# Kernel tuning notes

Hardware: AMD Instinct MI355X
Metric: run time of the kernel (lower is better)

The kernel has to match this reference:

```python
import jax, jax.numpy as jnp
import numpy as np

B, N, VF, EF, DV, DE, LN = 64, 64, 32, 16, 128, 128, 4
EPS_INNER = 128.0  # BatchNorm1d(MAX_N, internal_d_vert): 2nd positional arg is eps (faithful to source bug)
EPS_BN = 1e-5


def gev_layer(v_in, e_in, evW, evb, eW, eb, vW, vb, relu=True):
    act = jax.nn.relu if relu else (lambda x: x)
    ev = v_in @ evW + evb                                   # [B,N,De]
    # outer_v_sum: ev.unsqueeze(1) + ev.unsqueeze(2) -> [B,N,N,De]
    e_out = act(e_in @ eW + eb + ev[:, None, :, :] + ev[:, :, None, :])
    per_v_e = e_out.sum(axis=1)                             # sum-aggregate over dim 1
    v_out = act(jnp.concatenate([per_v_e, v_in], axis=-1) @ vW + vb)
    return v_out, e_out


def bn_flat(v, g, b):
    # BatchNorm1d(N*VF) on [B, N*VF] in training mode (biased var)
    x = v.reshape(-1, N * VF)
    mu = x.mean(axis=0)
    var = x.var(axis=0)
    x = (x - mu) * jax.lax.rsqrt(var + EPS_BN) * g + b
    return x.reshape(-1, N, VF)


def bn_inner(v, g, b):
    # BatchNorm1d(MAX_N, eps=128) on [B, N, D]: channels are the N axis, stats over (B, D)
    mu = v.mean(axis=(0, 2), keepdims=True)
    var = v.var(axis=(0, 2), keepdims=True)
    return (v - mu) * jax.lax.rsqrt(var + EPS_INNER) * g[None, :, None] + b[None, :, None]


def setup_inputs() -> dict:
    key = jax.random.key(0)
    ks = jax.random.split(key, 24)
    s = 0.01  # force_lin_init with init_noise=0.01, biases zero
    nrm = lambda k, shp: jax.random.normal(k, shp, dtype=jnp.float32) * s
    inp = {
        "v": jax.random.normal(ks[0], (B, N, VF), dtype=jnp.float32),
        "e": jax.random.normal(ks[1], (B, N, N, EF), dtype=jnp.float32),
        "bn_in_g": jnp.ones((N * VF,), jnp.float32),
        "bn_in_b": jnp.zeros((N * VF,), jnp.float32),
        "g1_evW": nrm(ks[2], (VF, DE)), "g1_evb": jnp.zeros((DE,), jnp.float32),
        "g1_eW": nrm(ks[3], (EF, DE)), "g1_eb": jnp.zeros((DE,), jnp.float32),
        "g1_vW": nrm(ks[4], (VF + DE, DV)), "g1_vb": jnp.zeros((DV,), jnp.float32),
        "inn_evW": nrm(ks[5], (LN, DV, DE)), "inn_evb": jnp.zeros((LN, DE), jnp.float32),
        "inn_eW": nrm(ks[6], (LN, DE, DE)), "inn_eb": jnp.zeros((LN, DE), jnp.float32),
        "inn_vW": nrm(ks[7], (LN, DV + DE, DV)), "inn_vb": jnp.zeros((LN, DV), jnp.float32),
        "bn_g": jnp.ones((LN, N), jnp.float32),
        "bn_b": jnp.zeros((LN, N), jnp.float32),
        "g3_evW": nrm(ks[8], (DV, 1)), "g3_evb": jnp.zeros((1,), jnp.float32),
        "g3_eW": nrm(ks[9], (DE, 1)), "g3_eb": jnp.zeros((1,), jnp.float32),
        "g3_vW": nrm(ks[10], (DV + 1, 1)), "g3_vb": jnp.zeros((1,), jnp.float32),
    }
    return inp


def reference(v, e, bn_in_g, bn_in_b, g1_evW, g1_evb, g1_eW, g1_eb, g1_vW, g1_vb,
              inn_evW, inn_evb, inn_eW, inn_eb, inn_vW, inn_vb, bn_g, bn_b,
              g3_evW, g3_evb, g3_eW, g3_eb, g3_vW, g3_vb):
    v = bn_flat(v, bn_in_g, bn_in_b)
    v, e = gev_layer(v, e, g1_evW, g1_evb, g1_eW, g1_eb, g1_vW, g1_vb)
    for i in range(LN):
        v_next, e_next = gev_layer(v, e, inn_evW[i], inn_evb[i], inn_eW[i], inn_eb[i], inn_vW[i], inn_vb[i])
        v = v_next + v  # resnet
        e = e_next + e
        v = bn_inner(v, bn_g[i], bn_b[i])
    v, e = gev_layer(v, e, g3_evW, g3_evb, g3_eW, g3_eb, g3_vW, g3_vb, relu=False)
    return v, e
```

## Files before the change

### kernel.cpp

```cpp
#include <hip/hip_runtime.h>
#include <hip/hip_bf16.h>


typedef __bf16 bf16_t;
typedef __bf16 bf16x8 __attribute__((ext_vector_type(8)));
typedef __bf16 bf16x4 __attribute__((ext_vector_type(4)));
typedef __bf16 bf16x2 __attribute__((ext_vector_type(2)));
typedef float f32x4 __attribute__((ext_vector_type(4)));

__device__ __forceinline__ void bar_lgkm() {
  asm volatile("s_waitcnt lgkmcnt(0)\n\ts_barrier" ::: "memory");
}

__device__ __forceinline__ unsigned pack2(float a, float b) {
  bf16_t ba = (bf16_t)a, bb = (bf16_t)b;
  unsigned short ua, ub;
  __builtin_memcpy(&ua, &ba, 2);
  __builtin_memcpy(&ub, &bb, 2);
  return (unsigned)ua | ((unsigned)ub << 16);
}
__device__ __forceinline__ float blo(unsigned u) {
  unsigned v = u << 16; float f; __builtin_memcpy(&f, &v, 4); return f;
}
__device__ __forceinline__ float bhi(unsigned u) {
  unsigned v = u & 0xffff0000u; float f; __builtin_memcpy(&f, &v, 4); return f;
}

__global__ __launch_bounds__(256) void k_prep(const float* __restrict__ vin,
    const float* __restrict__ g, const float* __restrict__ bt,
    const float* __restrict__ eW, const float* __restrict__ inn_vW,
    const float* __restrict__ g1_vW, const float* __restrict__ inn_evW,
    float* __restrict__ v0, bf16_t* __restrict__ Wt, float* __restrict__ stats,
    unsigned* __restrict__ vWp, unsigned* __restrict__ g1_vWp,
    unsigned* __restrict__ evWp, bf16_t* __restrict__ evWtB) {
  const int blk = blockIdx.x, tid = threadIdx.x;
  if (blk < 8) {
    int ch = blk * 256 + tid;
    float s = 0.f, s2 = 0.f;
    for (int b = 0; b < 64; ++b) { float x = vin[b * 2048 + ch]; s += x; s2 += x * x; }
    float mu = s * (1.f / 64.f);
    float var = s2 * (1.f / 64.f) - mu * mu;
    float sc = rsqrtf(var + 1e-5f) * g[ch];
    float bb = bt[ch];
    for (int b = 0; b < 64; ++b) {
      float x = vin[b * 2048 + ch];
      v0[b * 2048 + ch] = (x - mu) * sc + bb;
    }
  } else if (blk < 264) {
    int idx = (blk - 8) * 256 + tid;
    int l = idx >> 14, r = idx & 16383, n = r >> 7, k = r & 127;
    Wt[idx] = (bf16_t)eW[(l << 14) + (k << 7) + n];
  } else if (blk == 264) {
    for (int i = tid; i < 512; i += 256) stats[i] = 0.f;
  } else if (blk < 521) {
    int idx = (blk - 265) * 256 + tid;
    int l = idx >> 14, r = idx & 16383;
    int k8 = r >> 9, c = (r >> 2) & 127, j = r & 3;
    int ka = k8 * 8 + j * 2;
    vWp[idx] = pack2(inn_vW[(l << 15) + ka * 128 + c],
                     inn_vW[(l << 15) + (ka + 1) * 128 + c]);
  } else if (blk < 561) {
    int idx = (blk - 521) * 256 + tid;
    int k8 = idx >> 9, c = (idx >> 2) & 127, j = idx & 3;
    int ka = k8 * 8 + j * 2;
    g1_vWp[idx] = pack2(g1_vW[ka * 128 + c], g1_vW[(ka + 1) * 128 + c]);
  } else if (blk < 689) {
    int idx = (blk - 561) * 256 + tid;
    int l = idx >> 13, r = idx & 8191;
    int k8 = r >> 9, c = (r >> 2) & 127, j = r & 3;
    int ka = k8 * 8 + j * 2;
    evWp[idx] = pack2(inn_evW[(l << 14) + ka * 128 + c],
                      inn_evW[(l << 14) + (ka + 1) * 128 + c]);
  } else {
    int idx = (blk - 689) * 256 + tid;
    int l = idx >> 14, r = idx & 16383, n = r >> 7, k = r & 127;
    evWtB[idx] = (bf16_t)inn_evW[(l << 14) + (k << 7) + n];
  }
}

template <int K>
__global__ __launch_bounds__(256) void k_ev(const float* __restrict__ v_in,
    const float* __restrict__ W, const float* __restrict__ bias,
    float* __restrict__ out) {
  __shared__ float rows_s[8][K];
  const int r0 = blockIdx.x * 8;
  const int tid = threadIdx.x;
  const int c = tid & 127, h = tid >> 7;
  for (int idx = tid; idx < 8 * K; idx += 256) {
    int rr = idx / K, kk = idx % K;
    rows_s[rr][kk] = v_in[(r0 + rr) * K + kk];
  }
  __syncthreads();
  float acc[4];
  const float bv = bias[c];
#pragma unroll
  for (int r = 0; r < 4; ++r) acc[r] = bv;
  for (int k4 = 0; k4 < K; k4 += 4) {
    float w0 = W[(k4 + 0) * 128 + c], w1 = W[(k4 + 1) * 128 + c];
    float w2 = W[(k4 + 2) * 128 + c], w3 = W[(k4 + 3) * 128 + c];
#pragma unroll
    for (int r = 0; r < 4; ++r) {
      float4 x = *(const float4*)&rows_s[h * 4 + r][k4];
      acc[r] += x.x * w0 + x.y * w1 + x.z * w2 + x.w * w3;
    }
  }
#pragma unroll
  for (int r = 0; r < 4; ++r) out[(r0 + h * 4 + r) * 128 + c] = acc[r];
}

__global__ __launch_bounds__(256) void k_edge_g1(const float* __restrict__ e0,
    const float* __restrict__ eW, const float* __restrict__ eb,
    const float* __restrict__ evA, bf16_t* __restrict__ e_ws,
    const float* __restrict__ v0, const uint4* __restrict__ g1_vWp,
    const float* __restrict__ vb, const uint4* __restrict__ evW0p,
    const float* __restrict__ evb, float* __restrict__ v,
    float* __restrict__ evB) {
  __shared__ bf16_t A0s[2][64][40];
  __shared__ bf16_t Os[2][64][136];
  __shared__ float in_s[2][160];
  __shared__ float vr_s[2][128];
  __shared__ float red[2][2][128];
  const int b = blockIdx.x >> 5, j0 = (blockIdx.x & 31) * 2;
  const int tid = threadIdx.x;
  const int lane = tid & 63, w = tid >> 6;
  const int quad = lane >> 4, l16 = lane & 15;
  f32x4 v0reg;
  if (tid < 16)
    v0reg = *(const f32x4*)&v0[(b * 64 + j0 + (tid >> 3)) * 32 + (tid & 7) * 4];
#pragma unroll
  for (int t = 0; t < 2; ++t) {
    int idx = tid + t * 256;
    int row = idx >> 3, off = (idx & 7) * 4;
    int jc = off >> 4, k = off & 15;
    f32x4 x = *(const f32x4*)&e0[((b * 64 + row) * 64 + j0) * 16 + off];
    bf16x4 y;
#pragma unroll
    for (int r = 0; r < 4; ++r) y[r] = (bf16_t)x[r];
    *(bf16x4*)&A0s[jc][row][k] = y;
    bf16x4 z = {(bf16_t)0.f, (bf16_t)0.f, (bf16_t)0.f, (bf16_t)0.f};
    *(bf16x4*)&A0s[jc][row][16 + k] = z;
  }
  const int c0[2] = {w * 32 + quad * 4, w * 32 + 16 + quad * 4};
  bf16x8 wf[2];
#pragma unroll
  for (int nt = 0; nt < 2; ++nt) {
    const int c = w * 32 + nt * 16 + l16;
#pragma unroll
    for (int jj = 0; jj < 8; ++jj)
      wf[nt][jj] = (quad < 2) ? (bf16_t)eW[(quad * 8 + jj) * 128 + c] : (bf16_t)0.f;
  }
  f32x4 acc[2][4][2];
  {
    f32x4 ebv[2], evj[2][2], evi[4][2];
#pragma unroll
    for (int nt = 0; nt < 2; ++nt) {
      ebv[nt] = *(const f32x4*)&eb[c0[nt]];
#pragma unroll
      for (int jc = 0; jc < 2; ++jc)
        evj[jc][nt] = *(const f32x4*)&evA[(b * 64 + j0 + jc) * 128 + c0[nt]];
#pragma unroll
      for (int mt = 0; mt < 4; ++mt)
        evi[mt][nt] = *(const f32x4*)&evA[(b * 64 + mt * 16 + l16) * 128 + c0[nt]];
    }
#pragma unroll
    for (int jc = 0; jc < 2; ++jc)
#pragma unroll
      for (int mt = 0; mt < 4; ++mt)
#pragma unroll
        for (int nt = 0; nt < 2; ++nt)
          acc[jc][mt][nt] = ebv[nt] + evj[jc][nt] + evi[mt][nt];
  }
  __syncthreads();
#pragma unroll
  for (int jc = 0; jc < 2; ++jc) {
#pragma unroll
    for (int mt = 0; mt < 4; ++mt) {
      bf16x8 ef = *(const bf16x8*)&A0s[jc][mt * 16 + l16][quad * 8];
#pragma unroll
      for (int nt = 0; nt < 2; ++nt)
        acc[jc][mt][nt] = __builtin_amdgcn_mfma_f32_16x16x32_bf16(wf[nt], ef, acc[jc][mt][nt], 0, 0, 0);
    }
  }
#pragma unroll
  for (int jc = 0; jc < 2; ++jc) {
#pragma unroll
    for (int nt = 0; nt < 2; ++nt) {
      f32x4 ps = {0.f, 0.f, 0.f, 0.f};
#pragma unroll
      for (int mt = 0; mt < 4; ++mt) {
        const int i = mt * 16 + l16;
        bf16x4 outv;
#pragma unroll
        for (int r = 0; r < 4; ++r) {
          float vv = fmaxf(acc[jc][mt][nt][r], 0.f);
          ps[r] += vv;
          outv[r] = (bf16_t)vv;
        }
        *(bf16x4*)&Os[jc][i][c0[nt]] = outv;
      }
#pragma unroll
      for (int m = 1; m <= 8; m <<= 1) {
#pragma unroll
        for (int r = 0; r < 4; ++r) ps[r] += __shfl_xor(ps[r], m);
      }
      if (l16 == 0) *(f32x4*)&in_s[jc][c0[nt]] = ps;
    }
  }
  if (tid < 16) *(f32x4*)&in_s[tid >> 3][128 + (tid & 7) * 4] = v0reg;
  __syncthreads();
  {
    bf16_t* ebase = &e_ws[((size_t)(b * 64 + j0) * 64) * 128];
#pragma unroll
    for (int t = 0; t < 8; ++t) {
      int idx = tid + t * 256;
      *(int4*)&ebase[idx * 8] =
          *(const int4*)&Os[idx >> 10][(idx >> 4) & 63][(idx & 15) * 8];
    }
  }
  const int khalf = w >> 1, cbase = (w & 1) << 6;
  const int cc = cbase + lane;
  const int c = tid & 127, h = tid >> 7;
  {
    float p0 = 0.f, p1 = 0.f;
    const uint4* Wp = &g1_vWp[(khalf * 10) * 128 + cc];
    const float* xs0 = &in_s[0][khalf * 80];
    const float* xs1 = &in_s[1][khalf * 80];
#pragma unroll 5
    for (int k8 = 0; k8 < 10; ++k8) {
      uint4 wv = Wp[k8 * 128];
      float we0 = blo(wv.x), wo0 = bhi(wv.x);
      float we1 = blo(wv.y), wo1 = bhi(wv.y);
      float we2 = blo(wv.z), wo2 = bhi(wv.z);
      float we3 = blo(wv.w), wo3 = bhi(wv.w);
      float4 xa0 = *(const float4*)&xs0[k8 * 8];
      float4 xb0 = *(const float4*)&xs0[k8 * 8 + 4];
      float4 xa1 = *(const float4*)&xs1[k8 * 8];
      float4 xb1 = *(const float4*)&xs1[k8 * 8 + 4];
      p0 += xa0.x * we0 + xa0.y * wo0 + xa0.z * we1 + xa0.w * wo1
          + xb0.x * we2 + xb0.y * wo2 + xb0.z * we3 + xb0.w * wo3;
      p1 += xa1.x * we0 + xa1.y * wo0 + xa1.z * we1 + xa1.w * wo1
          + xb1.x * we2 + xb1.y * wo2 + xb1.z * we3 + xb1.w * wo3;
    }
    red[khalf][0][cc] = p0;
    red[khalf][1][cc] = p1;
  }
  bar_lgkm();
  {
    float vacc = vb[c] + red[0][h][c] + red[1][h][c];
    float vr = fmaxf(vacc, 0.f);
    v[(b * 64 + j0 + h) * 128 + c] = vr;
    vr_s[h][c] = vr;
  }
  bar_lgkm();
  {
    float p0 = 0.f, p1 = 0.f;
    const uint4* Wp = &evW0p[(khalf * 8) * 128 + cc];
    const float* xs0 = &vr_s[0][khalf << 6];
    const float* xs1 = &vr_s[1][khalf << 6];
#pragma unroll 4
    for (int k8 = 0; k8 < 8; ++k8) {
      uint4 wv = Wp[k8 * 128];
      float we0 = blo(wv.x), wo0 = bhi(wv.x);
      float we1 = blo(wv.y), wo1 = bhi(wv.y);
      float we2 = blo(wv.z), wo2 = bhi(wv.z);
      float we3 = blo(wv.w), wo3 = bhi(wv.w);
      float4 xa0 = *(const float4*)&xs0[k8 * 8];
      float4 xb0 = *(const float4*)&xs0[k8 * 8 + 4];
      float4 xa1 = *(const float4*)&xs1[k8 * 8];
      float4 xb1 = *(const float4*)&xs1[k8 * 8 + 4];
      p0 += xa0.x * we0 + xa0.y * wo0 + xa0.z * we1 + xa0.w * wo1
          + xb0.x * we2 + xb0.y * wo2 + xb0.z * we3 + xb0.w * wo3;
      p1 += xa1.x * we0 + xa1.y * wo0 + xa1.z * we1 + xa1.w * wo1
          + xb1.x * we2 + xb1.y * wo2 + xb1.z * we3 + xb1.w * wo3;
    }
    red[khalf][0][cc] = p0;
    red[khalf][1][cc] = p1;
  }
  bar_lgkm();
  evB[(b * 64 + j0 + h) * 128 + c] = evb[c] + red[0][h][c] + red[1][h][c];
}

template <bool LAST, bool EVGEN>
__global__ __launch_bounds__(256) void k_edge_inner(bf16_t* __restrict__ e_ws,
    const bf16_t* __restrict__ Wt, const float* __restrict__ eb,
    const float* __restrict__ ev, const float* __restrict__ eW3,
    float* __restrict__ edt, const float* __restrict__ vin,
    float* __restrict__ vout, const uint4* __restrict__ vWp,
    const float* __restrict__ vb, float* __restrict__ statsAcc,
    const float* __restrict__ statsPrev, const float* __restrict__ gPrev,
    const float* __restrict__ btPrev, const bf16_t* __restrict__ evWtB,
    const float* __restrict__ evb) {
  __shared__ bf16_t As[2][64][136];
  __shared__ float W3s[128];
  __shared__ float in_s[2][256];
  __shared__ float red[2][2][128];
  __shared__ float part[4][2];
  __shared__ float scs[64], shs[64];
  const int b = blockIdx.x >> 5, j0 = (blockIdx.x & 31) * 2;
  const int tid = threadIdx.x;
  const int lane = tid & 63, w = tid >> 6;
  const int quad = lane >> 4, l16 = lane & 15;
  bf16_t* ebase = &e_ws[((size_t)(b * 64 + j0) * 64) * 128];
  int4 stg[8];
#pragma unroll
  for (int t = 0; t < 8; ++t) {
    int idx = tid + t * 256;
    stg[t] = *(const int4*)&ebase[idx * 8];
  }
  f32x4 vreg;
  if (tid < 64)
    vreg = *(const f32x4*)&vin[(b * 64 + j0 + (tid >> 5)) * 128 + (tid & 31) * 4];
  if (LAST) {
    if (tid < 128) W3s[tid] = eW3[tid];
  }
  bf16x8 wf[2][4];
#pragma unroll
  for (int nt = 0; nt < 2; ++nt)
#pragma unroll
    for (int ks = 0; ks < 4; ++ks)
      wf[nt][ks] = *(const bf16x8*)&Wt[(w * 32 + nt * 16 + l16) * 128 + ks * 32 + quad * 8];
  const int c0[2] = {w * 32 + quad * 4, w * 32 + 16 + quad * 4};
  f32x4 acc[2][4][2];
  if (EVGEN) {
    if (tid < 64) {
      float mu = statsPrev[tid] * (1.f / 8192.f);
      float var = statsPrev[64 + tid] * (1.f / 8192.f) - mu * mu;
      float sc = rsqrtf(var + 128.f) * gPrev[tid];
      scs[tid] = sc;
      shs[tid] = btPrev[tid] - mu * sc;
    }
    bf16x8 wf2[2][4];
#pragma unroll
    for (int nt = 0; nt < 2; ++nt)
#pragma unroll
      for (int ks = 0; ks < 4; ++ks)
        wf2[nt][ks] = *(const bf16x8*)&evWtB[(w * 32 + nt * 16 + l16) * 128 + ks * 32 + quad * 8];
    bar_lgkm();
#pragma unroll
    for (int t = 0; t < 16; ++t) {
      int row = t * 4 + w;
      float2 xv = *(const float2*)&vin[(b * 64 + row) * 128 + lane * 2];
      float sc = scs[row], sh = shs[row];
      bf16x2 o;
      o[0] = (bf16_t)(xv.x * sc + sh);
      o[1] = (bf16_t)(xv.y * sc + sh);
      *(bf16x2*)&As[0][row][lane * 2] = o;
    }
    if (tid < 64) {
      int rr = j0 + (tid >> 5);
      vreg = vreg * scs[rr] + shs[rr];
    }
    bar_lgkm();
    f32x4 acc_ev[4][2];
#pragma unroll
    for (int nt = 0; nt < 2; ++nt) {
      f32x4 bias = *(const f32x4*)&evb[c0[nt]];
#pragma unroll
      for (int mt = 0; mt < 4; ++mt) acc_ev[mt][nt] = bias;
    }
#pragma unroll
    for (int ks = 0; ks < 4; ++ks) {
      bf16x8 bfm[4];
#pragma unroll
      for (int mt = 0; mt < 4; ++mt)
        bfm[mt] = *(const bf16x8*)&As[0][mt * 16 + l16][ks * 32 + quad * 8];
#pragma unroll
      for (int mt = 0; mt < 4; ++mt)
#pragma unroll
        for (int nt = 0; nt < 2; ++nt)
          acc_ev[mt][nt] = __builtin_amdgcn_mfma_f32_16x16x32_bf16(wf2[nt][ks], bfm[mt], acc_ev[mt][nt], 0, 0, 0);
    }
    const int mtj = j0 >> 4;
    f32x4 evrow[2];
#pragma unroll
    for (int mt = 0; mt < 4; ++mt)
      if (mtj == mt) { evrow[0] = acc_ev[mt][0]; evrow[1] = acc_ev[mt][1]; }
    f32x4 evj[2][2];
#pragma unroll
    for (int jc = 0; jc < 2; ++jc) {
      int src = (quad << 4) | ((j0 + jc) & 15);
#pragma unroll
      for (int nt = 0; nt < 2; ++nt)
#pragma unroll
        for (int r = 0; r < 4; ++r)
          evj[jc][nt][r] = __shfl(evrow[nt][r], src);
    }
#pragma unroll
    for (int nt = 0; nt < 2; ++nt) {
      f32x4 ebv = *(const f32x4*)&eb[c0[nt]];
#pragma unroll
      for (int jc = 0; jc < 2; ++jc)
#pragma unroll
        for (int mt = 0; mt < 4; ++mt)
          acc[jc][mt][nt] = ebv + evj[jc][nt] + acc_ev[mt][nt];
    }
    bar_lgkm();
  } else {
    f32x4 ebv[2], evj[2][2], evi[4][2];
#pragma unroll
    for (int nt = 0; nt < 2; ++nt) {
      ebv[nt] = *(const f32x4*)&eb[c0[nt]];
#pragma unroll
      for (int jc = 0; jc < 2; ++jc)
        evj[jc][nt] = *(const f32x4*)&ev[(b * 64 + j0 + jc) * 128 + c0[nt]];
#pragma unroll
      for (int mt = 0; mt < 4; ++mt)
        evi[mt][nt] = *(const f32x4*)&ev[(b * 64 + mt * 16 + l16) * 128 + c0[nt]];
    }
#pragma unroll
    for (int jc = 0; jc < 2; ++jc)
#pragma unroll
      for (int mt = 0; mt < 4; ++mt)
#pragma unroll
        for (int nt = 0; nt < 2; ++nt)
          acc[jc][mt][nt] = ebv[nt] + evj[jc][nt] + evi[mt][nt];
  }
#pragma unroll
  for (int t = 0; t < 8; ++t) {
    int idx = tid + t * 256;
    *(int4*)&As[idx >> 10][(idx >> 4) & 63][(idx & 15) * 8] = stg[t];
  }
  bar_lgkm();
#pragma unroll
  for (int ks = 0; ks < 4; ++ks) {
    bf16x8 ef[2][4];
#pragma unroll
    for (int jc = 0; jc < 2; ++jc)
#pragma unroll
      for (int mt = 0; mt < 4; ++mt)
        ef[jc][mt] = *(const bf16x8*)&As[jc][mt * 16 + l16][ks * 32 + quad * 8];
#pragma unroll
    for (int jc = 0; jc < 2; ++jc)
#pragma unroll
      for (int mt = 0; mt < 4; ++mt)
#pragma unroll
        for (int nt = 0; nt < 2; ++nt)
          acc[jc][mt][nt] = __builtin_amdgcn_mfma_f32_16x16x32_bf16(wf[nt][ks], ef[jc][mt], acc[jc][mt][nt], 0, 0, 0);
  }
  bar_lgkm();
#pragma unroll
  for (int jc = 0; jc < 2; ++jc) {
#pragma unroll
    for (int nt = 0; nt < 2; ++nt) {
      f32x4 ps = {0.f, 0.f, 0.f, 0.f};
#pragma unroll
      for (int mt = 0; mt < 4; ++mt) {
        const int i = mt * 16 + l16;
        bf16x4 eo = *(const bf16x4*)&As[jc][i][c0[nt]];
        bf16x4 outv;
#pragma unroll
        for (int r = 0; r < 4; ++r) {
          float vv = fmaxf(acc[jc][mt][nt][r], 0.f);
          ps[r] += vv;
          outv[r] = (bf16_t)(vv + (float)eo[r]);
        }
        *(bf16x4*)&As[jc][i][c0[nt]] = outv;
      }
#pragma unroll
      for (int m = 1; m <= 8; m <<= 1) {
#pragma unroll
        for (int r = 0; r < 4; ++r) ps[r] += __shfl_xor(ps[r], m);
      }
      if (l16 == 0) *(f32x4*)&in_s[jc][c0[nt]] = ps;
    }
  }
  if (tid < 64) *(f32x4*)&in_s[tid >> 5][128 + (tid & 31) * 4] = vreg;
  bar_lgkm();
  const int khalf = w >> 1, cbase = (w & 1) << 6;
  const int cc = cbase + lane;
  float p0 = 0.f, p1 = 0.f;
  {
    const uint4* Wp = &vWp[(khalf * 16) * 128 + cc];
    const float* xs0 = &in_s[0][khalf << 7];
    const float* xs1 = &in_s[1][khalf << 7];
#pragma unroll 4
    for (int k8 = 0; k8 < 16; ++k8) {
      uint4 wv = Wp[k8 * 128];
      float we0 = blo(wv.x), wo0 = bhi(wv.x);
      float we1 = blo(wv.y), wo1 = bhi(wv.y);
      float we2 = blo(wv.z), wo2 = bhi(wv.z);
      float we3 = blo(wv.w), wo3 = bhi(wv.w);
      float4 xa0 = *(const float4*)&xs0[k8 * 8];
      float4 xb0 = *(const float4*)&xs0[k8 * 8 + 4];
      float4 xa1 = *(const float4*)&xs1[k8 * 8];
      float4 xb1 = *(const float4*)&xs1[k8 * 8 + 4];
      p0 += xa0.x * we0 + xa0.y * wo0 + xa0.z * we1 + xa0.w * wo1
          + xb0.x * we2 + xb0.y * wo2 + xb0.z * we3 + xb0.w * wo3;
      p1 += xa1.x * we0 + xa1.y * wo0 + xa1.z * we1 + xa1.w * wo1
          + xb1.x * we2 + xb1.y * wo2 + xb1.z * we3 + xb1.w * wo3;
    }
  }
  if (!LAST) {
#pragma unroll
    for (int t = 0; t < 8; ++t) {
      int idx = tid + t * 256;
      *(int4*)&ebase[idx * 8] =
          *(const int4*)&As[idx >> 10][(idx >> 4) & 63][(idx & 15) * 8];
    }
  } else {
    const int i = tid >> 2, q = tid & 3;
#pragma unroll
    for (int jc = 0; jc < 2; ++jc) {
      float d = 0.f;
#pragma unroll
      for (int t = 0; t < 4; ++t) {
        bf16x8 x = *(const bf16x8*)&As[jc][i][q * 32 + t * 8];
#pragma unroll
        for (int u = 0; u < 8; ++u) d += (float)x[u] * W3s[q * 32 + t * 8 + u];
      }
      d += __shfl_xor(d, 1);
      d += __shfl_xor(d, 2);
      if (q == 0) edt[(b * 64 + j0 + jc) * 64 + i] = d;
    }
  }
  red[khalf][0][cc] = p0;
  red[khalf][1][cc] = p1;
  bar_lgkm();
  const int c = tid & 127, h = tid >> 7;
  float vacc = vb[c] + red[0][h][c] + red[1][h][c];
  float vnew = fmaxf(vacc, 0.f) + in_s[h][128 + c];
  vout[(b * 64 + j0 + h) * 128 + c] = vnew;
  float s = vnew, s2 = vnew * vnew;
#pragma unroll
  for (int m = 1; m <= 32; m <<= 1) {
    s += __shfl_xor(s, m);
    s2 += __shfl_xor(s2, m);
  }
  if (lane == 0) { part[w][0] = s; part[w][1] = s2; }
  bar_lgkm();
  if (tid < 2) {
    int n = j0 + tid;
    atomicAdd(&statsAcc[n], part[tid * 2][0] + part[tid * 2 + 1][0]);
    atomicAdd(&statsAcc[64 + n], part[tid * 2][1] + part[tid * 2 + 1][1]);
  }
}

__global__ __launch_bounds__(256) void k_g3(const float* __restrict__ vv,
    const float* __restrict__ stats3, const float* __restrict__ g,
    const float* __restrict__ bt, const float* __restrict__ evW3,
    const float* __restrict__ evb3, const float* __restrict__ eb3,
    const float* __restrict__ edt, const float* __restrict__ vW3,
    const float* __restrict__ vb3, float* __restrict__ out_v,
    float* __restrict__ out_e) {
  __shared__ float vbn[64][132];
  __shared__ float edts[64][68];
  __shared__ float scs[64], shs[64];
  __shared__ float W3e[128];
  __shared__ float vWs[132];
  __shared__ float ev3s[64];
  __shared__ float pj[4][64];
  const int b = blockIdx.x, tid = threadIdx.x;
  if (tid < 64) {
    float mu = stats3[tid] * (1.f / 8192.f);
    float var = stats3[64 + tid] * (1.f / 8192.f) - mu * mu;
    float sc = rsqrtf(var + 128.f) * g[tid];
    scs[tid] = sc;
    shs[tid] = bt[tid] - mu * sc;
  }
  if (tid < 128) W3e[tid] = evW3[tid];
  if (tid < 129) vWs[tid] = vW3[tid];
  __syncthreads();
#pragma unroll
  for (int t = 0; t < 8; ++t) {
    int idx = t * 1024 + tid * 4;
    int row = idx >> 7, cc = idx & 127;
    f32x4 x = *(const f32x4*)&vv[(b * 64 + row) * 128 + cc];
    *(f32x4*)&vbn[row][cc] = x * scs[row] + shs[row];
  }
#pragma unroll
  for (int t = 0; t < 4; ++t) {
    int idx = t * 1024 + tid * 4;
    int j = idx >> 6, i = idx & 63;
    *(f32x4*)&edts[j][i] = *(const f32x4*)&edt[(b * 64 + j) * 64 + i];
  }
  __syncthreads();
  {
    int i = tid >> 2, q = tid & 3;
    float d = 0.f;
#pragma unroll
    for (int u = 0; u < 32; ++u) d += vbn[i][q * 32 + u] * W3e[q * 32 + u];
    d += __shfl_xor(d, 1);
    d += __shfl_xor(d, 2);
    if (q == 0) ev3s[i] = d + evb3[0];
  }
  __syncthreads();
  {
    int q = tid >> 6, j = tid & 63;
    float s = 0.f;
    const float e3 = eb3[0];
    const float evj = ev3s[j];
#pragma unroll
    for (int r = 0; r < 16; ++r) {
      int i = q * 16 + r;
      float val = edts[j][i] + e3 + ev3s[i] + evj;
      out_e[(b * 64 + i) * 64 + j] = val;
      s += val;
    }
    pj[q][j] = s;
  }
  __syncthreads();
  {
    int n = tid >> 2, q = tid & 3;
    float d = 0.f;
#pragma unroll
    for (int u = 0; u < 32; ++u) d += vbn[n][q * 32 + u] * vWs[1 + q * 32 + u];
    d += __shfl_xor(d, 1);
    d += __shfl_xor(d, 2);
    if (q == 0) {
      float p3 = pj[0][n] + pj[1][n] + pj[2][n] + pj[3][n];
      out_v[b * 64 + n] = d + p3 * vWs[0] + vb3[0];
    }
  }
}

extern "C" void kernel_launch(void* const* d_in, const int* in_sizes, int n_in,
                              void* d_out, int out_size, void* d_ws, size_t ws_size,
                              hipStream_t stream) {
  const float* in_v    = (const float*)d_in[0];
  const float* in_e    = (const float*)d_in[1];
  const float* bn_in_g = (const float*)d_in[2];
  const float* bn_in_b = (const float*)d_in[3];
  const float* g1_evW  = (const float*)d_in[4];
  const float* g1_evb  = (const float*)d_in[5];
  const float* g1_eW   = (const float*)d_in[6];
  const float* g1_eb   = (const float*)d_in[7];
  const float* g1_vW   = (const float*)d_in[8];
  const float* g1_vb   = (const float*)d_in[9];
  const float* inn_evW = (const float*)d_in[10];
  const float* inn_evb = (const float*)d_in[11];
  const float* inn_eW  = (const float*)d_in[12];
  const float* inn_eb  = (const float*)d_in[13];
  const float* inn_vW  = (const float*)d_in[14];
  const float* inn_vb  = (const float*)d_in[15];
  const float* bn_g    = (const float*)d_in[16];
  const float* bn_b    = (const float*)d_in[17];
  const float* g3_evW  = (const float*)d_in[18];
  const float* g3_evb  = (const float*)d_in[19];
  const float* g3_eW   = (const float*)d_in[20];
  const float* g3_eb   = (const float*)d_in[21];
  const float* g3_vW   = (const float*)d_in[22];
  const float* g3_vb   = (const float*)d_in[23];

  char* ws = (char*)d_ws;
  bf16_t* e_ws = (bf16_t*)(ws);
  float* vA       = (float*)(ws + 67108864);
  float* evA      = (float*)(ws + 69206016);
  float* evB      = (float*)(ws + 71303168);
  float* v0       = (float*)(ws + 73400320);
  bf16_t* Wt      = (bf16_t*)(ws + 73924608);
  float* edt      = (float*)(ws + 74055680);
  float* stats    = (float*)(ws + 75104256);
  unsigned* vWp   = (unsigned*)(ws + 75106304);
  unsigned* g1_vWp= (unsigned*)(ws + 75368448);
  unsigned* evWp  = (unsigned*)(ws + 75409408);
  bf16_t* evWtB   = (bf16_t*)(ws + 75540480);
  float* vB       = (float*)(ws + 75671552);

  float* out_v = (float*)d_out;
  float* out_e = (float*)d_out + 4096;

  k_prep<<<945, 256, 0, stream>>>(in_v, bn_in_g, bn_in_b, inn_eW, inn_vW, g1_vW,
                                  inn_evW, v0, Wt, stats, vWp, g1_vWp, evWp, evWtB);

  k_ev<32><<<512, 256, 0, stream>>>(v0, g1_evW, g1_evb, evA);
  k_edge_g1<<<2048, 256, 0, stream>>>(in_e, g1_eW, g1_eb, evA, e_ws,
                                      v0, (const uint4*)g1_vWp, g1_vb,
                                      (const uint4*)evWp, inn_evb, vA, evB);

  float* vbufs[2] = {vA, vB};
  for (int l = 0; l < 4; ++l) {
    float* vin_l  = vbufs[l & 1];
    float* vout_l = vbufs[(l + 1) & 1];
    if (l == 0)
      k_edge_inner<false, false><<<2048, 256, 0, stream>>>(e_ws, Wt,
          inn_eb, evB, g3_eW, edt, vin_l, vout_l,
          (const uint4*)vWp, inn_vb, stats,
          nullptr, nullptr, nullptr, nullptr, nullptr);
    else if (l < 3)
      k_edge_inner<false, true><<<2048, 256, 0, stream>>>(e_ws, Wt + l * 16384,
          inn_eb + l * 128, evB, g3_eW, edt, vin_l, vout_l,
          (const uint4*)vWp + l * 4096, inn_vb + l * 128, stats + l * 128,
          stats + (l - 1) * 128, bn_g + (l - 1) * 64, bn_b + (l - 1) * 64,
          evWtB + l * 16384, inn_evb + l * 128);
    else
      k_edge_inner<true, true><<<2048, 256, 0, stream>>>(e_ws, Wt + l * 16384,
          inn_eb + l * 128, evB, g3_eW, edt, vin_l, vout_l,
          (const uint4*)vWp + l * 4096, inn_vb + l * 128, stats + l * 128,
          stats + (l - 1) * 128, bn_g + (l - 1) * 64, bn_b + (l - 1) * 64,
          evWtB + l * 16384, inn_evb + l * 128);
  }

  k_g3<<<64, 256, 0, stream>>>(vA, stats + 384, bn_g + 192, bn_b + 192,
                               g3_evW, g3_evb, g3_eb, edt, g3_vW, g3_vb,
                               out_v, out_e);
}
```

Baseline: 367.5 us.

## Process four j-rows per block with software-pipelined edge tile loads

Measured after the change: 376.1 us. +2.3%, slower.

```diff
diff --git a/kernel.cpp b/kernel.cpp
--- a/kernel.cpp
+++ b/kernel.cpp
@@ -281,7 +281,7 @@
 }
 
 template <bool LAST, bool EVGEN>
-__global__ __launch_bounds__(256) void k_edge_inner(bf16_t* __restrict__ e_ws,
+__global__ __launch_bounds__(256, 2) void k_edge_inner(bf16_t* __restrict__ e_ws,
     const bf16_t* __restrict__ Wt, const float* __restrict__ eb,
     const float* __restrict__ ev, const float* __restrict__ eW3,
     float* __restrict__ edt, const float* __restrict__ vin,
@@ -290,25 +290,24 @@
     const float* __restrict__ statsPrev, const float* __restrict__ gPrev,
     const float* __restrict__ btPrev, const bf16_t* __restrict__ evWtB,
     const float* __restrict__ evb) {
-  __shared__ bf16_t As[2][64][136];
+  __shared__ bf16_t As[2][2][64][136];
   __shared__ float W3s[128];
-  __shared__ float in_s[2][256];
+  __shared__ float in_s[2][2][256];
   __shared__ float red[2][2][128];
   __shared__ float part[4][2];
   __shared__ float scs[64], shs[64];
-  const int b = blockIdx.x >> 5, j0 = (blockIdx.x & 31) * 2;
+  const int b = blockIdx.x >> 4, j0 = (blockIdx.x & 15) * 4;
   const int tid = threadIdx.x;
   const int lane = tid & 63, w = tid >> 6;
   const int quad = lane >> 4, l16 = lane & 15;
-  bf16_t* ebase = &e_ws[((size_t)(b * 64 + j0) * 64) * 128];
+  bf16_t* ebase0 = &e_ws[((size_t)(b * 64 + j0) * 64) * 128];
+  bf16_t* ebase1 = ebase0 + 2 * 64 * 128;
   int4 stg[8];
 #pragma unroll
-  for (int t = 0; t < 8; ++t) {
-    int idx = tid + t * 256;
-    stg[t] = *(const int4*)&ebase[idx * 8];
-  }
+  for (int t = 0; t < 8; ++t)
+    stg[t] = *(const int4*)&ebase0[(tid + t * 256) * 8];
   f32x4 vreg;
-  if (tid < 64)
+  if (tid < 128)
     vreg = *(const f32x4*)&vin[(b * 64 + j0 + (tid >> 5)) * 128 + (tid & 31) * 4];
   if (LAST) {
     if (tid < 128) W3s[tid] = eW3[tid];
@@ -320,7 +319,11 @@
     for (int ks = 0; ks < 4; ++ks)
       wf[nt][ks] = *(const bf16x8*)&Wt[(w * 32 + nt * 16 + l16) * 128 + ks * 32 + quad * 8];
   const int c0[2] = {w * 32 + quad * 4, w * 32 + 16 + quad * 4};
-  f32x4 acc[2][4][2];
+  f32x4 ebv[2];
+#pragma unroll
+  for (int nt = 0; nt < 2; ++nt) ebv[nt] = *(const f32x4*)&eb[c0[nt]];
+  f32x4 acc_ev[4][2];
+  f32x4 evj[4][2];
   if (EVGEN) {
     if (tid < 64) {
       float mu = statsPrev[tid] * (1.f / 8192.f);
@@ -344,14 +347,13 @@
       bf16x2 o;
       o[0] = (bf16_t)(xv.x * sc + sh);
       o[1] = (bf16_t)(xv.y * sc + sh);
-      *(bf16x2*)&As[0][row][lane * 2] = o;
-    }
-    if (tid < 64) {
+      *(bf16x2*)&As[1][1][row][lane * 2] = o;
+    }
+    if (tid < 128) {
       int rr = j0 + (tid >> 5);
       vreg = vreg * scs[rr] + shs[rr];
     }
     bar_lgkm();
-    f32x4 acc_ev[4][2];
 #pragma unroll
     for (int nt = 0; nt < 2; ++nt) {
       f32x4 bias = *(const f32x4*)&evb[c0[nt]];
@@ -363,7 +365,7 @@
       bf16x8 bfm[4];
 #pragma unroll
       for (int mt = 0; mt < 4; ++mt)
-        bfm[mt] = *(const bf16x8*)&As[0][mt * 16 + l16][ks * 32 + quad * 8];
+        bfm[mt] = *(const bf16x8*)&As[1][1][mt * 16 + l16][ks * 32 + quad * 8];
 #pragma unroll
       for (int mt = 0; mt < 4; ++mt)
 #pragma unroll
@@ -375,51 +377,42 @@
 #pragma unroll
     for (int mt = 0; mt < 4; ++mt)
       if (mtj == mt) { evrow[0] = acc_ev[mt][0]; evrow[1] = acc_ev[mt][1]; }
-    f32x4 evj[2][2];
-#pragma unroll
-    for (int jc = 0; jc < 2; ++jc) {
-      int src = (quad << 4) | ((j0 + jc) & 15);
+#pragma unroll
+    for (int jj = 0; jj < 4; ++jj) {
+      int src = (quad << 4) | ((j0 + jj) & 15);
 #pragma unroll
       for (int nt = 0; nt < 2; ++nt)
 #pragma unroll
         for (int r = 0; r < 4; ++r)
-          evj[jc][nt][r] = __shfl(evrow[nt][r], src);
-    }
+          evj[jj][nt][r] = __shfl(evrow[nt][r], src);
+    }
+  } else {
 #pragma unroll
     for (int nt = 0; nt < 2; ++nt) {
-      f32x4 ebv = *(const f32x4*)&eb[c0[nt]];
-#pragma unroll
-      for (int jc = 0; jc < 2; ++jc)
-#pragma unroll
-        for (int mt = 0; mt < 4; ++mt)
-          acc[jc][mt][nt] = ebv + evj[jc][nt] + acc_ev[mt][nt];
-    }
-    bar_lgkm();
-  } else {
-    f32x4 ebv[2], evj[2][2], evi[4][2];
-#pragma unroll
-    for (int nt = 0; nt < 2; ++nt) {
-      ebv[nt] = *(const f32x4*)&eb[c0[nt]];
-#pragma unroll
-      for (int jc = 0; jc < 2; ++jc)
-        evj[jc][nt] = *(const f32x4*)&ev[(b * 64 + j0 + jc) * 128 + c0[nt]];
-#pragma unroll
-      for (int mt = 0; mt < 4; ++mt)
-        evi[mt][nt] = *(const f32x4*)&ev[(b * 64 + mt * 16 + l16) * 128 + c0[nt]];
-    }
-#pragma unroll
-    for (int jc = 0; jc < 2; ++jc)
-#pragma unroll
-      for (int mt = 0; mt < 4; ++mt)
-#pragma unroll
-        for (int nt = 0; nt < 2; ++nt)
-          acc[jc][mt][nt] = ebv[nt] + evj[jc][nt] + evi[mt][nt];
+#pragma unroll
+      for (int jj = 0; jj < 4; ++jj)
+        evj[jj][nt] = *(const f32x4*)&ev[(b * 64 + j0 + jj) * 128 + c0[nt]];
+#pragma unroll
+      for (int mt = 0; mt < 4; ++mt)
+        acc_ev[mt][nt] = *(const f32x4*)&ev[(b * 64 + mt * 16 + l16) * 128 + c0[nt]];
+    }
   }
 #pragma unroll
   for (int t = 0; t < 8; ++t) {
     int idx = tid + t * 256;
-    *(int4*)&As[idx >> 10][(idx >> 4) & 63][(idx & 15) * 8] = stg[t];
-  }
+    *(int4*)&As[0][idx >> 10][(idx >> 4) & 63][(idx & 15) * 8] = stg[t];
+  }
+#pragma unroll
+  for (int t = 0; t < 8; ++t)
+    stg[t] = *(const int4*)&ebase1[(tid + t * 256) * 8];
+  f32x4 acc[2][4][2];
+#pragma unroll
+  for (int jc = 0; jc < 2; ++jc)
+#pragma unroll
+    for (int mt = 0; mt < 4; ++mt)
+#pragma unroll
+      for (int nt = 0; nt < 2; ++nt)
+        acc[jc][mt][nt] = ebv[nt] + evj[jc][nt] + acc_ev[mt][nt];
   bar_lgkm();
 #pragma unroll
   for (int ks = 0; ks < 4; ++ks) {
@@ -428,7 +421,7 @@
     for (int jc = 0; jc < 2; ++jc)
 #pragma unroll
       for (int mt = 0; mt < 4; ++mt)
-        ef[jc][mt] = *(const bf16x8*)&As[jc][mt * 16 + l16][ks * 32 + quad * 8];
+        ef[jc][mt] = *(const bf16x8*)&As[0][jc][mt * 16 + l16][ks * 32 + quad * 8];
 #pragma unroll
     for (int jc = 0; jc < 2; ++jc)
 #pragma unroll
@@ -446,7 +439,7 @@
 #pragma unroll
       for (int mt = 0; mt < 4; ++mt) {
         const int i = mt * 16 + l16;
-        bf16x4 eo = *(const bf16x4*)&As[jc][i][c0[nt]];
+        bf16x4 eo = *(const bf16x4*)&As[0][jc][i][c0[nt]];
         bf16x4 outv;
 #pragma unroll
         for (int r = 0; r < 4; ++r) {
@@ -454,84 +447,160 @@
           ps[r] += vv;
           outv[r] = (bf16_t)(vv + (float)eo[r]);
         }
-        *(bf16x4*)&As[jc][i][c0[nt]] = outv;
+        *(bf16x4*)&As[0][jc][i][c0[nt]] = outv;
       }
 #pragma unroll
       for (int m = 1; m <= 8; m <<= 1) {
 #pragma unroll
         for (int r = 0; r < 4; ++r) ps[r] += __shfl_xor(ps[r], m);
       }
-      if (l16 == 0) *(f32x4*)&in_s[jc][c0[nt]] = ps;
-    }
-  }
-  if (tid < 64) *(f32x4*)&in_s[tid >> 5][128 + (tid & 31) * 4] = vreg;
+      if (l16 == 0) *(f32x4*)&in_s[0][jc][c0[nt]] = ps;
+    }
+  }
+  bar_lgkm();
+  if (!LAST) {
+#pragma unroll
+    for (int t = 0; t < 8; ++t) {
+      int idx = tid + t * 256;
+      *(int4*)&ebase0[idx * 8] =
+          *(const int4*)&As[0][idx >> 10][(idx >> 4) & 63][(idx & 15) * 8];
+    }
+  }
+#pragma unroll
+  for (int t = 0; t < 8; ++t) {
+    int idx = tid + t * 256;
+    *(int4*)&As[1][idx >> 10][(idx >> 4) & 63][(idx & 15) * 8] = stg[t];
+  }
+#pragma unroll
+  for (int jc = 0; jc < 2; ++jc)
+#pragma unroll
+    for (int mt = 0; mt < 4; ++mt)
+#pragma unroll
+      for (int nt = 0; nt < 2; ++nt)
+        acc[jc][mt][nt] = ebv[nt] + evj[2 + jc][nt] + acc_ev[mt][nt];
+  bar_lgkm();
+#pragma unroll
+  for (int ks = 0; ks < 4; ++ks) {
+    bf16x8 ef[2][4];
+#pragma unroll
+    for (int jc = 0; jc < 2; ++jc)
+#pragma unroll
+      for (int mt = 0; mt < 4; ++mt)
+        ef[jc][mt] = *(const bf16x8*)&As[1][jc][mt * 16 + l16][ks * 32 + quad * 8];
+#pragma unroll
+    for (int jc = 0; jc < 2; ++jc)
+#pragma unroll
+      for (int mt = 0; mt < 4; ++mt)
+#pragma unroll
+        for (int nt = 0; nt < 2; ++nt)
+          acc[jc][mt][nt] = __builtin_amdgcn_mfma_f32_16x16x32_bf16(wf[nt][ks], ef[jc][mt], acc[jc][mt][nt], 0, 0, 0);
+  }
+  bar_lgkm();
+#pragma unroll
+  for (int jc = 0; jc < 2; ++jc) {
+#pragma unroll
+    for (int nt = 0; nt < 2; ++nt) {
+      f32x4 ps = {0.f, 0.f, 0.f, 0.f};
+#pragma unroll
+      for (int mt = 0; mt < 4; ++mt) {
+        const int i = mt * 16 + l16;
+        bf16x4 eo = *(const bf16x4*)&As[1][jc][i][c0[nt]];
+        bf16x4 outv;
+#pragma unroll
+        for (int r = 0; r < 4; ++r) {
+          float vv = fmaxf(acc[jc][mt][nt][r], 0.f);
+          ps[r] += vv;
+          outv[r] = (bf16_t)(vv + (float)eo[r]);
+        }
+        *(bf16x4*)&As[1][jc][i][c0[nt]] = outv;
+      }
+#pragma unroll
+      for (int m = 1; m <= 8; m <<= 1) {
+#pragma unroll
+        for (int r = 0; r < 4; ++r) ps[r] += __shfl_xor(ps[r], m);
+      }
+      if (l16 == 0) *(f32x4*)&in_s[1][jc][c0[nt]] = ps;
+    }
+  }
+  bar_lgkm();
+  if (!LAST) {
+#pragma unroll
+    for (int t = 0; t < 8; ++t) {
+      int idx = tid + t * 256;
+      *(int4*)&ebase1[idx * 8] =
+          *(const int4*)&As[1][idx >> 10][(idx >> 4) & 63][(idx & 15) * 8];
+    }
+  } else {
+    const int i = tid >> 2, q = tid & 3;
+#pragma unroll
+    for (int p = 0; p < 2; ++p) {
+#pragma unroll
+      for (int jc = 0; jc < 2; ++jc) {
+        float d = 0.f;
+#pragma unroll
+        for (int t = 0; t < 4; ++t) {
+          bf16x8 x = *(const bf16x8*)&As[p][jc][i][q * 32 + t * 8];
+#pragma unroll
+          for (int u = 0; u < 8; ++u) d += (float)x[u] * W3s[q * 32 + t * 8 + u];
+        }
+        d += __shfl_xor(d, 1);
+        d += __shfl_xor(d, 2);
+        if (q == 0) edt[(b * 64 + j0 + p * 2 + jc) * 64 + i] = d;
+      }
+    }
+  }
+  if (tid < 128) {
+    int row = tid >> 5;
+    *(f32x4*)&in_s[row >> 1][row & 1][128 + (tid & 31) * 4] = vreg;
+  }
   bar_lgkm();
   const int khalf = w >> 1, cbase = (w & 1) << 6;
   const int cc = cbase + lane;
-  float p0 = 0.f, p1 = 0.f;
-  {
-    const uint4* Wp = &vWp[(khalf * 16) * 128 + cc];
-    const float* xs0 = &in_s[0][khalf << 7];
-    const float* xs1 = &in_s[1][khalf << 7];
+  const int c = tid & 127, h = tid >> 7;
+#pragma unroll
+  for (int p = 0; p < 2; ++p) {
+    float p0 = 0.f, p1 = 0.f;
+    {
+      const uint4* Wp = &vWp[(khalf * 16) * 128 + cc];
+      const float* xs0 = &in_s[p][0][khalf << 7];
+      const float* xs1 = &in_s[p][1][khalf << 7];
 #pragma unroll 4
-    for (int k8 = 0; k8 < 16; ++k8) {
-      uint4 wv = Wp[k8 * 128];
-      float we0 = blo(wv.x), wo0 = bhi(wv.x);
-      float we1 = blo(wv.y), wo1 = bhi(wv.y);
-      float we2 = blo(wv.z), wo2 = bhi(wv.z);
-      float we3 = blo(wv.w), wo3 = bhi(wv.w);
-      float4 xa0 = *(const float4*)&xs0[k8 * 8];
-      float4 xb0 = *(const float4*)&xs0[k8 * 8 + 4];
-      float4 xa1 = *(const float4*)&xs1[k8 * 8];
-      float4 xb1 = *(const float4*)&xs1[k8 * 8 + 4];
-      p0 += xa0.x * we0 + xa0.y * wo0 + xa0.z * we1 + xa0.w * wo1
-          + xb0.x * we2 + xb0.y * wo2 + xb0.z * we3 + xb0.w * wo3;
-      p1 += xa1.x * we0 + xa1.y * wo0 + xa1.z * we1 + xa1.w * wo1
-          + xb1.x * we2 + xb1.y * wo2 + xb1.z * we3 + xb1.w * wo3;
-    }
-  }
-  if (!LAST) {
-#pragma unroll
-    for (int t = 0; t < 8; ++t) {
-      int idx = tid + t * 256;
-      *(int4*)&ebase[idx * 8] =
-          *(const int4*)&As[idx >> 10][(idx >> 4) & 63][(idx & 15) * 8];
-    }
-  } else {
-    const int i = tid >> 2, q = tid & 3;
-#pragma unroll
-    for (int jc = 0; jc < 2; ++jc) {
-      float d = 0.f;
-#pragma unroll
-      for (int t = 0; t < 4; ++t) {
-        bf16x8 x = *(const bf16x8*)&As[jc][i][q * 32 + t * 8];
-#pragma unroll
-        for (int u = 0; u < 8; ++u) d += (float)x[u] * W3s[q * 32 + t * 8 + u];
+      for (int k8 = 0; k8 < 16; ++k8) {
+        uint4 wv = Wp[k8 * 128];
+        float we0 = blo(wv.x), wo0 = bhi(wv.x);
+        float we1 = blo(wv.y), wo1 = bhi(wv.y);
+        float we2 = blo(wv.z), wo2 = bhi(wv.z);
+        float we3 = blo(wv.w), wo3 = bhi(wv.w);
+        float4 xa0 = *(const float4*)&xs0[k8 * 8];
+        float4 xb0 = *(const float4*)&xs0[k8 * 8 + 4];
+        float4 xa1 = *(const float4*)&xs1[k8 * 8];
+        float4 xb1 = *(const float4*)&xs1[k8 * 8 + 4];
+        p0 += xa0.x * we0 + xa0.y * wo0 + xa0.z * we1 + xa0.w * wo1
+            + xb0.x * we2 + xb0.y * wo2 + xb0.z * we3 + xb0.w * wo3;
+        p1 += xa1.x * we0 + xa1.y * wo0 + xa1.z * we1 + xa1.w * wo1
+            + xb1.x * we2 + xb1.y * wo2 + xb1.z * we3 + xb1.w * wo3;
       }
-      d += __shfl_xor(d, 1);
-      d += __shfl_xor(d, 2);
-      if (q == 0) edt[(b * 64 + j0 + jc) * 64 + i] = d;
-    }
-  }
-  red[khalf][0][cc] = p0;
-  red[khalf][1][cc] = p1;
-  bar_lgkm();
-  const int c = tid & 127, h = tid >> 7;
-  float vacc = vb[c] + red[0][h][c] + red[1][h][c];
-  float vnew = fmaxf(vacc, 0.f) + in_s[h][128 + c];
-  vout[(b * 64 + j0 + h) * 128 + c] = vnew;
-  float s = vnew, s2 = vnew * vnew;
-#pragma unroll
-  for (int m = 1; m <= 32; m <<= 1) {
-    s += __shfl_xor(s, m);
-    s2 += __shfl_xor(s2, m);
-  }
-  if (lane == 0) { part[w][0] = s; part[w][1] = s2; }
-  bar_lgkm();
-  if (tid < 2) {
-    int n = j0 + tid;
-    atomicAdd(&statsAcc[n], part[tid * 2][0] + part[tid * 2 + 1][0]);
-    atomicAdd(&statsAcc[64 + n], part[tid * 2][1] + part[tid * 2 + 1][1]);
+    }
+    red[khalf][0][cc] = p0;
+    red[khalf][1][cc] = p1;
+    bar_lgkm();
+    float vacc = vb[c] + red[0][h][c] + red[1][h][c];
+    float vnew = fmaxf(vacc, 0.f) + in_s[p][h][128 + c];
+    vout[(b * 64 + j0 + p * 2 + h) * 128 + c] = vnew;
+    float s = vnew, s2 = vnew * vnew;
+#pragma unroll
+    for (int m = 1; m <= 32; m <<= 1) {
+      s += __shfl_xor(s, m);
+      s2 += __shfl_xor(s2, m);
+    }
+    if (lane == 0) { part[w][0] = s; part[w][1] = s2; }
+    bar_lgkm();
+    if (tid < 2) {
+      int n = j0 + p * 2 + tid;
+      atomicAdd(&statsAcc[n], part[tid * 2][0] + part[tid * 2 + 1][0]);
+      atomicAdd(&statsAcc[64 + n], part[tid * 2][1] + part[tid * 2 + 1][1]);
+    }
+    if (p == 0) bar_lgkm();
   }
 }
 
@@ -672,18 +741,18 @@
     float* vin_l  = vbufs[l & 1];
     float* vout_l = vbufs[(l + 1) & 1];
     if (l == 0)
-      k_edge_inner<false, false><<<2048, 256, 0, stream>>>(e_ws, Wt,
+      k_edge_inner<false, false><<<1024, 256, 0, stream>>>(e_ws, Wt,
           inn_eb, evB, g3_eW, edt, vin_l, vout_l,
           (const uint4*)vWp, inn_vb, stats,
           nullptr, nullptr, nullptr, nullptr, nullptr);
     else if (l < 3)
-      k_edge_inner<false, true><<<2048, 256, 0, stream>>>(e_ws, Wt + l * 16384,
+      k_edge_inner<false, true><<<1024, 256, 0, stream>>>(e_ws, Wt + l * 16384,
           inn_eb + l * 128, evB, g3_eW, edt, vin_l, vout_l,
           (const uint4*)vWp + l * 4096, inn_vb + l * 128, stats + l * 128,
           stats + (l - 1) * 128, bn_g + (l - 1) * 64, bn_b + (l - 1) * 64,
           evWtB + l * 16384, inn_evb + l * 128);
     else
-      k_edge_inner<true, true><<<2048, 256, 0, stream>>>(e_ws, Wt + l * 16384,
+      k_edge_inner<true, true><<<1024, 256, 0, stream>>>(e_ws, Wt + l * 16384,
           inn_eb + l * 128, evB, g3_eW, edt, vin_l, vout_l,
           (const uint4*)vWp + l * 4096, inn_vb + l * 128, stats + l * 128,
           stats + (l - 1) * 128, bn_g + (l - 1) * 64, bn_b + (l - 1) * 64,
```
